# Kernel tuning notes

Measured on AMD Instinct MI355X. Metric: run time of the kernel, lower is better.

Reference implementation:

```python
import jax, jax.numpy as jnp
import numpy as np

N = 1024      # num_waves
L = 32        # latent_dim
H = 64        # hidden_dim
EPS = 1e-6
SELF_SCALE = 0.5
INT_SCALE = 0.3


def _xavier(k, shape, gain=0.5):
    fan_out, fan_in = shape
    std = gain * np.sqrt(2.0 / (fan_in + fan_out))
    return (jax.random.normal(k, shape, jnp.float32) * std).astype(jnp.float32)


def setup_inputs() -> dict:
    key = jax.random.key(0)
    ks = jax.random.split(key, 12)
    d = {}
    d['state'] = jax.random.normal(ks[0], (N * (L + 1),), jnp.float32)
    # SelfDynamicsNetwork: L->H->H->L, tanh, xavier_normal gain=0.5, zero bias
    d['Ws1'] = _xavier(ks[1], (H, L)); d['bs1'] = jnp.zeros((H,), jnp.float32)
    d['Ws2'] = _xavier(ks[2], (H, H)); d['bs2'] = jnp.zeros((H,), jnp.float32)
    d['Ws3'] = _xavier(ks[3], (L, H)); d['bs3'] = jnp.zeros((L,), jnp.float32)
    # InteractionNetwork: 4L->H->H->L
    d['Wi1'] = _xavier(ks[4], (H, 4 * L)); d['bi1'] = jnp.zeros((H,), jnp.float32)
    d['Wi2'] = _xavier(ks[5], (H, H));     d['bi2'] = jnp.zeros((H,), jnp.float32)
    d['Wi3'] = _xavier(ks[6], (L, H));     d['bi3'] = jnp.zeros((L,), jnp.float32)
    # QuantumPhaseMixer
    d['phase_w'] = jax.random.normal(ks[7], (L,), jnp.float32) * 0.1
    d['Wc'] = _xavier(ks[8], (L, 2 * L), gain=1.0)
    d['bc'] = jnp.zeros((L,), jnp.float32)
    # per-wave aggressiveness
    d['aggr'] = jnp.ones((N,), jnp.float32) * 0.5
    return d


def reference(state, Ws1, bs1, Ws2, bs2, Ws3, bs3,
              Wi1, bi1, Wi2, bi2, Wi3, bi3,
              phase_w, Wc, bc, aggr):
    s = state.reshape(N, L + 1)
    h = s[:, :L]          # [N, L]
    phases = s[:, L]      # [N]

    def mlp(x, W1, b1, W2, b2, W3, b3):
        x = jnp.tanh(x @ W1.T + b1)
        x = jnp.tanh(x @ W2.T + b2)
        return x @ W3.T + b3

    self_term = mlp(h, Ws1, bs1, Ws2, bs2, Ws3, bs3)   # [N, L]
    dh = self_term  # prev_state is None -> estimated velocity = self_dynamics(h)

    # pairwise distance factor
    diff = h[:, None, :] - h[None, :, :]                # [N, N, L] (h_i - h_j)
    dist = jnp.linalg.norm(diff, axis=-1) + EPS         # [N, N]
    dfac = jnp.minimum(1.0 / dist, 2.0)

    # InteractionNetwork on concat([h_i, h_j, dh_i, dh_j]): split first layer
    a_i = h @ Wi1[:, :L].T + dh @ Wi1[:, 2 * L:3 * L].T           # [N, H]
    b_j = h @ Wi1[:, L:2 * L].T + dh @ Wi1[:, 3 * L:].T + bi1    # [N, H]
    x1 = jnp.tanh(a_i[:, None, :] + b_j[None, :, :])              # [N, N, H]
    x2 = jnp.tanh(x1 @ Wi2.T + bi2)                               # [N, N, H]
    k_ij = x2 @ Wi3.T + bi3                                       # [N, N, L]

    # QuantumPhaseMixer
    phase_diff = phases[:, None] - phases[None, :]                # [N, N]
    pf = jnp.cos(phase_diff[..., None] * phase_w)                 # [N, N, L]
    coh = jax.nn.sigmoid((h @ Wc[:, :L].T)[:, None, :]
                         + (h @ Wc[:, L:].T)[None, :, :] + bc)    # [N, N, L]
    quantum = pf * coh * (-diff)                                  # h_j - h_i = -diff

    agg = jax.nn.sigmoid(aggr)                                    # [N]
    inter = dfac[..., None] * k_ij * agg[:, None, None] + quantum # [N, N, L]
    mask = 1.0 - jnp.eye(N, dtype=inter.dtype)                    # skip j == i
    isum = jnp.einsum('ijl,ij->il', inter, mask)                  # sum over j

    # env is None -> speed_mults = 1, refractions = 0
    dh_dt = SELF_SCALE * self_term + INT_SCALE * isum
    dphase = 0.1 + 0.05 * jnp.sum(jnp.abs(isum), axis=-1)
    return jnp.concatenate([dh_dt, dphase[:, None]], axis=1).reshape(-1)
```

## Files before the change

### kernel.cpp

```cpp
#include <hip/hip_runtime.h>
#include <hip/hip_bf16.h>
#include <math.h>

#define NN 1024
#define LDIM 32
#define HDIM 64

#define WS_SELF 0
#define WS_AA   (WS_SELF + NN*LDIM)
#define WS_CI   (WS_AA   + NN*HDIM)
#define WS_AGG  (WS_CI   + NN*LDIM)
#define WS_BI2  (WS_AGG  + NN)
#define WS_BI3  (WS_BI2  + HDIM)
#define WS_FEND (WS_BI3  + LDIM)

#define U_BJB  0
#define U_HJB  (U_BJB + NN*HDIM)
#define U_JT   (U_HJB + NN*LDIM)
#define U_W2B  (U_JT  + NN*LDIM*4)
#define U_W3B  (U_W2B + HDIM*HDIM)
#define U_END  (U_W3B + LDIM*HDIM)

#define PK_W1  0
#define PK_W2  1024
#define PK_W3  3072
#define PK_WI1 4096
#define PK_WC  8192
#define PK_END 9216

#define K2P  2.88539008f
#define K1N  (-1.44269504f)

typedef __attribute__((ext_vector_type(8))) short bf16x8;
typedef __attribute__((ext_vector_type(4))) float f32x4;

__device__ __forceinline__ float fast_rcp(float x) { return __builtin_amdgcn_rcpf(x); }
__device__ __forceinline__ float fast_tanh(float x) {
    float e = __builtin_amdgcn_exp2f(x * K2P);
    return 1.0f - 2.0f * fast_rcp(e + 1.0f);
}
__device__ __forceinline__ float tanh_pre(float xp) {
    return 1.0f - 2.0f * fast_rcp(__builtin_amdgcn_exp2f(xp) + 1.0f);
}
__device__ __forceinline__ float fast_sigmoid(float x) {
    return fast_rcp(1.0f + __builtin_amdgcn_exp2f(x * K1N));
}
__device__ __forceinline__ float blo(unsigned int u) { union { unsigned int i; float f; } v; v.i = u << 16; return v.f; }
__device__ __forceinline__ float bhi(unsigned int u) { union { unsigned int i; float f; } v; v.i = u & 0xffff0000u; return v.f; }
__device__ __forceinline__ float bf2f(unsigned short u) { union { unsigned int i; float f; } v; v.i = ((unsigned int)u) << 16; return v.f; }
__device__ __forceinline__ unsigned short f2bf(float f) {
    __hip_bfloat16 b = __float2bfloat16(f);
    unsigned short u; __builtin_memcpy(&u, &b, 2); return u;
}
__device__ __forceinline__ unsigned int pk2(float a, float b) {
    float2 t; t.x = a; t.y = b;
    __hip_bfloat162 h = __float22bfloat162_rn(t);
    unsigned int u; __builtin_memcpy(&u, &h, 4); return u;
}

__global__ __launch_bounds__(256) void precompute(
    const float* __restrict__ state,
    const float* __restrict__ Ws1, const float* __restrict__ bs1,
    const float* __restrict__ Ws2, const float* __restrict__ bs2,
    const float* __restrict__ Ws3, const float* __restrict__ bs3,
    const float* __restrict__ Wi1, const float* __restrict__ bi1,
    const float* __restrict__ Wi2, const float* __restrict__ bi2,
    const float* __restrict__ Wi3, const float* __restrict__ bi3,
    const float* __restrict__ phw, const float* __restrict__ Wc,
    const float* __restrict__ bc,  const float* __restrict__ aggr,
    float* __restrict__ ws, unsigned short* __restrict__ wsu) {
    const int tid = threadIdx.x;
    const int w = tid >> 6, t = tid & 63;
    const int i = blockIdx.x * 4 + w;

    __shared__ unsigned int wlds[PK_END];
    __shared__ float shh[4][32], shdh[4][32], sht1[4][64], sht2[4][64];
    __shared__ float shph[4];

    {
        const float2* s1 = (const float2*)Ws1;
        #pragma unroll
        for (int r = 0; r < 4; r++) { int e = tid + r * 256; int f = e >> 4, k2 = e & 15;
            float2 v = s1[e]; wlds[PK_W1 + k2 * 64 + f] = pk2(v.x, v.y); }
        const float2* s2 = (const float2*)Ws2;
        #pragma unroll
        for (int r = 0; r < 8; r++) { int e = tid + r * 256; int f = e >> 5, k2 = e & 31;
            float2 v = s2[e]; wlds[PK_W2 + k2 * 64 + f] = pk2(v.x, v.y); }
        const float2* s3 = (const float2*)Ws3;
        #pragma unroll
        for (int r = 0; r < 4; r++) { int e = tid + r * 256; int f = e >> 5, k2 = e & 31;
            float2 v = s3[e]; wlds[PK_W3 + k2 * 32 + f] = pk2(v.x, v.y); }
        const float2* si = (const float2*)Wi1;
        #pragma unroll
        for (int r = 0; r < 16; r++) { int e = tid + r * 256; int f = e >> 6, c2 = e & 63;
            float2 v = si[e]; wlds[PK_WI1 + c2 * 64 + f] = pk2(v.x, v.y); }
        const float2* sc = (const float2*)Wc;
        #pragma unroll
        for (int r = 0; r < 4; r++) { int e = tid + r * 256; int f = e >> 5, c2 = e & 31;
            float2 v = sc[e]; wlds[PK_WC + c2 * 32 + f] = pk2(v.x, v.y); }
    }
    if (blockIdx.x == 0) {
        #pragma unroll
        for (int r = 0; r < 16; r++) { int e = tid + r * 256; wsu[U_W2B + e] = f2bf(Wi2[e] * K2P); }
        #pragma unroll
        for (int r = 0; r < 8; r++)  { int e = tid + r * 256; wsu[U_W3B + e] = f2bf(Wi3[e]); }
        if (tid < HDIM) ws[WS_BI2 + tid] = bi2[tid] * K2P;
        if (tid < LDIM) ws[WS_BI3 + tid] = bi3[tid];
    }

    float sv = (t < 33) ? state[i * 33 + t] : 0.f;
    if (t < 32) shh[w][t] = sv;
    if (t == 32) shph[w] = sv;
    if (t == 33) ws[WS_AGG + i] = fast_sigmoid(aggr[i]);
    __syncthreads();

    {
        float s = bs1[t];
        const unsigned int* W = wlds + PK_W1;
        #pragma unroll
        for (int k2 = 0; k2 < 16; k2++) {
            unsigned int p = W[k2 * 64 + t];
            s = fmaf(blo(p), shh[w][2 * k2], s);
            s = fmaf(bhi(p), shh[w][2 * k2 + 1], s);
        }
        sht1[w][t] = fast_tanh(s);
    }
    __syncthreads();
    {
        float s = bs2[t];
        const unsigned int* W = wlds + PK_W2;
        #pragma unroll
        for (int k2 = 0; k2 < 32; k2++) {
            unsigned int p = W[k2 * 64 + t];
            s = fmaf(blo(p), sht1[w][2 * k2], s);
            s = fmaf(bhi(p), sht1[w][2 * k2 + 1], s);
        }
        sht2[w][t] = fast_tanh(s);
    }
    __syncthreads();
    if (t < 32) {
        float s = bs3[t];
        const unsigned int* W = wlds + PK_W3;
        #pragma unroll
        for (int k2 = 0; k2 < 32; k2++) {
            unsigned int p = W[k2 * 32 + t];
            s = fmaf(blo(p), sht2[w][2 * k2], s);
            s = fmaf(bhi(p), sht2[w][2 * k2 + 1], s);
        }
        ws[WS_SELF + i * 32 + t] = s;
        shdh[w][t] = s;
    }
    __syncthreads();
    {
        float sa = 0.f, sb = bi1[t];
        const unsigned int* W = wlds + PK_WI1;
        #pragma unroll
        for (int k2 = 0; k2 < 16; k2++) {
            float h0 = shh[w][2 * k2], h1 = shh[w][2 * k2 + 1];
            float d0 = shdh[w][2 * k2], d1 = shdh[w][2 * k2 + 1];
            unsigned int wa  = W[k2 * 64 + t];
            unsigned int wb  = W[(16 + k2) * 64 + t];
            unsigned int wa2 = W[(32 + k2) * 64 + t];
            unsigned int wb2 = W[(48 + k2) * 64 + t];
            sa = fmaf(blo(wa), h0, sa);  sa = fmaf(bhi(wa), h1, sa);
            sb = fmaf(blo(wb), h0, sb);  sb = fmaf(bhi(wb), h1, sb);
            sa = fmaf(blo(wa2), d0, sa); sa = fmaf(bhi(wa2), d1, sa);
            sb = fmaf(blo(wb2), d0, sb); sb = fmaf(bhi(wb2), d1, sb);
        }
        ws[WS_AA + i * 64 + t]  = sa * K2P;
        wsu[U_BJB + i * 64 + t] = f2bf(sb * K2P);
    }
    if (t < 32) {
        float si = 0.f, sj = 0.f;
        const unsigned int* W = wlds + PK_WC;
        #pragma unroll
        for (int m2 = 0; m2 < 16; m2++) {
            float h0 = shh[w][2 * m2], h1 = shh[w][2 * m2 + 1];
            unsigned int wi = W[m2 * 32 + t];
            unsigned int wj = W[(16 + m2) * 32 + t];
            si = fmaf(blo(wi), h0, si); si = fmaf(bhi(wi), h1, si);
            sj = fmaf(blo(wj), h0, sj); sj = fmaf(bhi(wj), h1, sj);
        }
        ws[WS_CI + i * 32 + t] = (si + bc[t]) * K1N;
        float h = shh[w][t];
        wsu[U_HJB + i * 32 + t] = f2bf(h);
        float sc, cc;
        __sincosf(shph[w] * phw[t], &sc, &cc);
        uint2 jt; jt.x = pk2(h, sj * K1N); jt.y = pk2(cc, sc);
        *(uint2*)(wsu + U_JT + (i * 32 + t) * 4) = jt;
    }
}

__global__ __launch_bounds__(256) void pair_kernel(
    const float* __restrict__ ws, const unsigned short* __restrict__ wsu,
    float* __restrict__ out) {
    const int i    = blockIdx.x;
    const int tid  = threadIdx.x;
    const int w    = tid >> 6;
    const int lane = tid & 63;
    const int q    = lane >> 4;
    const int m    = lane & 15;
    const int jw   = w * 16;
    const int sub  = lane & 3;

    __shared__ unsigned short W2ls[64 * 72];
    __shared__ unsigned short W3ls[32 * 72];
    __shared__ unsigned short x2ls[4 * 2 * 16 * 72];
    __shared__ float aLS[64];
    __shared__ float redT[4][32], redU[4][32], redV[4][32];
    __shared__ float sfw[4];

    if (tid < 64) aLS[tid] = ws[WS_AA + i * 64 + tid];
    {
        int row = tid >> 2, c = (tid & 3) * 16;
        const uint4* s2 = (const uint4*)(wsu + U_W2B + row * 64 + c);
        uint4 d0 = s2[0], d1 = s2[1];
        uint4* dd = (uint4*)(&W2ls[row * 72 + c]);
        dd[0] = d0; dd[1] = d1;
        if (row < 32) {
            const uint4* s3 = (const uint4*)(wsu + U_W3B + row * 64 + c);
            uint4 e0 = s3[0], e1 = s3[1];
            uint4* d3 = (uint4*)(&W3ls[row * 72 + c]);
            d3[0] = e0; d3[1] = e1;
        }
    }
    float hi8[8];
    {
        uint4 hv4 = *(const uint4*)(wsu + U_HJB + i * 32 + sub * 8);
        unsigned int hd[4] = {hv4.x, hv4.y, hv4.z, hv4.w};
        #pragma unroll
        for (int e = 0; e < 4; e++) { hi8[2 * e] = blo(hd[e]); hi8[2 * e + 1] = bhi(hd[e]); }
    }
    f32x4 b2q[4];
    #pragma unroll
    for (int nb = 0; nb < 4; nb++) {
        float4 bv = *(const float4*)(ws + WS_BI2 + nb * 16 + q * 4);
        b2q[nb][0] = bv.x; b2q[nb][1] = bv.y; b2q[nb][2] = bv.z; b2q[nb][3] = bv.w;
    }
    float hiv[2], cibv[2];
    #pragma unroll
    for (int lb = 0; lb < 2; lb++) {
        int l = lb * 16 + m;
        hiv[lb]  = bf2f(wsu[U_HJB + i * 32 + l]);
        cibv[lb] = ws[WS_CI + i * 32 + l];
    }
    const float aggi = ws[WS_AGG + i];
    const float sub0 = (sub == 0) ? 1.0f : 0.0f;

    const unsigned short* hp = wsu + U_HJB + (jw + (lane >> 2)) * 32 + sub * 8;
    const unsigned short* bp = wsu + U_BJB + (jw + m) * 64 + q * 8;
    const unsigned short* jp = wsu + U_JT + ((jw + q * 4) * 32 + m) * 4;

    uint4 hvA = *(const uint4*)hp;
    uint4 b0A = *(const uint4*)bp;
    uint4 b1A = *(const uint4*)(bp + 32);
    uint4 hvB, b0B, b1B;
    __syncthreads();

    f32x4 accK[2];
    #pragma unroll
    for (int lb = 0; lb < 2; lb++) { accK[lb][0]=0.f; accK[lb][1]=0.f; accK[lb][2]=0.f; accK[lb][3]=0.f; }
    float aU[2] = {0.f, 0.f}, aV[2] = {0.f, 0.f};
    float sumfac = 0.f;

    unsigned short* xb0 = &x2ls[w * 2 * 1152];
    unsigned short* xb1 = xb0 + 1152;

    auto stageB = [&](const unsigned short* xb) {
        bf16x8 x2f[2];
        #pragma unroll
        for (int s = 0; s < 2; s++)
            x2f[s] = *(const bf16x8*)(&xb[m * 72 + s * 32 + q * 8]);
        #pragma unroll
        for (int lb = 0; lb < 2; lb++) {
            #pragma unroll
            for (int s = 0; s < 2; s++) {
                bf16x8 w3f = *(const bf16x8*)(&W3ls[(lb * 16 + m) * 72 + s * 32 + q * 8]);
                accK[lb] = __builtin_amdgcn_mfma_f32_16x16x32_bf16(x2f[s], w3f, accK[lb], 0, 0, 0);
            }
        }
    };

    auto body = [&](int T, uint4 hvc, uint4 b0c, uint4 b1c,
                    uint4& hvn, uint4& b0n, uint4& b1n,
                    unsigned short* xcur, const unsigned short* xprev) {
        hp += 2048; bp += 4096;
        hvn = *(const uint4*)hp;
        b0n = *(const uint4*)bp;
        b1n = *(const uint4*)(bp + 32);
        uint2 jt[8];
        #pragma unroll
        for (int r = 0; r < 4; r++) {
            jt[r]     = *(const uint2*)(jp + r * 128);
            jt[4 + r] = *(const uint2*)(jp + 64 + r * 128);
        }
        jp += 8192;

        if (T > 0) stageB(xprev);

        float facm;
        {
            unsigned int hd[4] = {hvc.x, hvc.y, hvc.z, hvc.w};
            float s = 0.f;
            #pragma unroll
            for (int e = 0; e < 4; e++) {
                float d0 = hi8[2 * e]     - blo(hd[e]);
                float d1 = hi8[2 * e + 1] - bhi(hd[e]);
                s = fmaf(d0, d0, s); s = fmaf(d1, d1, s);
            }
            s += __shfl_xor(s, 1); s += __shfl_xor(s, 2);
            int jj = T * 64 + jw + (lane >> 2);
            float facown = fminf(__builtin_amdgcn_rsqf(s), 2.0f) * aggi;
            facown = (jj == i) ? 0.0f : facown;
            sumfac = fmaf(sub0, facown, sumfac);
            facm = __shfl(facown, 4 * m);
        }
        const float fm2 = -2.0f * facm;

        bf16x8 afr[2];
        {
            unsigned int bd[8] = {b0c.x, b0c.y, b0c.z, b0c.w, b1c.x, b1c.y, b1c.z, b1c.w};
            #pragma unroll
            for (int s = 0; s < 2; s++) {
                union { uint4 u4; bf16x8 v; } pkd;
                #pragma unroll
                for (int e = 0; e < 4; e++) {
                    const float* ab = &aLS[s * 32 + q * 8 + 2 * e];
                    float x0 = tanh_pre(ab[0] + blo(bd[s * 4 + e]));
                    float x1 = tanh_pre(ab[1] + bhi(bd[s * 4 + e]));
                    ((unsigned int*)&pkd.u4)[e] = pk2(x0, x1);
                }
                afr[s] = pkd.v;
            }
        }

        f32x4 accA[4];
        #pragma unroll
        for (int nb = 0; nb < 4; nb++) {
            f32x4 acc = b2q[nb];
            #pragma unroll
            for (int s = 0; s < 2; s++) {
                bf16x8 w2f = *(const bf16x8*)(&W2ls[(nb * 16 + m) * 72 + s * 32 + q * 8]);
                acc = __builtin_amdgcn_mfma_f32_16x16x32_bf16(w2f, afr[s], acc, 0, 0, 0);
            }
            accA[nb] = acc;
        }
        #pragma unroll
        for (int nb = 0; nb < 4; nb++) {
            float r0 = fast_rcp(__builtin_amdgcn_exp2f(accA[nb][0]) + 1.0f);
            float r1 = fast_rcp(__builtin_amdgcn_exp2f(accA[nb][1]) + 1.0f);
            float r2 = fast_rcp(__builtin_amdgcn_exp2f(accA[nb][2]) + 1.0f);
            float r3 = fast_rcp(__builtin_amdgcn_exp2f(accA[nb][3]) + 1.0f);
            float t0 = fmaf(fm2, r0, facm), t1 = fmaf(fm2, r1, facm);
            float t2 = fmaf(fm2, r2, facm), t3 = fmaf(fm2, r3, facm);
            uint2 pk; pk.x = pk2(t0, t1); pk.y = pk2(t2, t3);
            *(uint2*)(&xcur[m * 72 + nb * 16 + q * 4]) = pk;
        }

        #pragma unroll
        for (int lb = 0; lb < 2; lb++) {
            float u = 0.f, v = 0.f;
            #pragma unroll
            for (int r = 0; r < 4; r++) {
                uint2 jv = jt[lb * 4 + r];
                float hj = blo(jv.x), cj = bhi(jv.x);
                float pjc = blo(jv.y), pjs = bhi(jv.y);
                float coh = fast_rcp(1.0f + __builtin_amdgcn_exp2f(cibv[lb] + cj));
                float cd  = coh * (hiv[lb] - hj);
                u = fmaf(cd, pjc, u);
                v = fmaf(cd, pjs, v);
            }
            aU[lb] += u; aV[lb] += v;
        }
    };

    #pragma unroll 1
    for (int T = 0; T < 16; T += 2) {
        body(T,     hvA, b0A, b1A, hvB, b0B, b1B, xb0, xb1);
        body(T + 1, hvB, b0B, b1B, hvA, b0A, b1A, xb1, xb0);
    }
    stageB(xb1);

    float T1[2];
    #pragma unroll
    for (int lb = 0; lb < 2; lb++) {
        T1[lb] = (accK[lb][0] + accK[lb][1]) + (accK[lb][2] + accK[lb][3]);
        T1[lb] += __shfl_xor(T1[lb], 16); T1[lb] += __shfl_xor(T1[lb], 32);
        aU[lb] += __shfl_xor(aU[lb], 16); aU[lb] += __shfl_xor(aU[lb], 32);
        aV[lb] += __shfl_xor(aV[lb], 16); aV[lb] += __shfl_xor(aV[lb], 32);
    }
    sumfac += __shfl_xor(sumfac, 1);  sumfac += __shfl_xor(sumfac, 2);
    sumfac += __shfl_xor(sumfac, 4);  sumfac += __shfl_xor(sumfac, 8);
    sumfac += __shfl_xor(sumfac, 16); sumfac += __shfl_xor(sumfac, 32);
    if (lane < 16) {
        redT[w][m] = T1[0];      redT[w][16 + m] = T1[1];
        redU[w][m] = aU[0];      redU[w][16 + m] = aU[1];
        redV[w][m] = aV[0];      redV[w][16 + m] = aV[1];
    }
    if (lane == 0) sfw[w] = sumfac;
    __syncthreads();
    if (tid < 32) {
        int l = tid;
        float t1 = (redT[0][l] + redT[1][l]) + (redT[2][l] + redT[3][l]);
        float uu = (redU[0][l] + redU[1][l]) + (redU[2][l] + redU[3][l]);
        float vv = (redV[0][l] + redV[1][l]) + (redV[2][l] + redV[3][l]);
        float sf = (sfw[0] + sfw[1]) + (sfw[2] + sfw[3]);
        uint2 jti = *(const uint2*)(wsu + U_JT + (i * 32 + l) * 4);
        float pic = blo(jti.y), pis = bhi(jti.y);
        float isum = t1 + sf * ws[WS_BI3 + l] - (pic * uu + pis * vv);
        out[i * 33 + l] = 0.5f * ws[WS_SELF + i * 32 + l] + 0.3f * isum;
        redT[0][l] = fabsf(isum);
    }
    __syncthreads();
    if (tid == 0) {
        float s = 0.f;
        #pragma unroll
        for (int l = 0; l < 32; l++) s += redT[0][l];
        out[i * 33 + 32] = 0.1f + 0.05f * s;
    }
}

extern "C" void kernel_launch(void* const* d_in, const int* in_sizes, int n_in,
                              void* d_out, int out_size, void* d_ws, size_t ws_size,
                              hipStream_t stream) {
    const float* state   = (const float*)d_in[0];
    const float* Ws1     = (const float*)d_in[1];
    const float* bs1     = (const float*)d_in[2];
    const float* Ws2     = (const float*)d_in[3];
    const float* bs2     = (const float*)d_in[4];
    const float* Ws3     = (const float*)d_in[5];
    const float* bs3     = (const float*)d_in[6];
    const float* Wi1     = (const float*)d_in[7];
    const float* bi1     = (const float*)d_in[8];
    const float* Wi2     = (const float*)d_in[9];
    const float* bi2     = (const float*)d_in[10];
    const float* Wi3     = (const float*)d_in[11];
    const float* bi3     = (const float*)d_in[12];
    const float* phase_w = (const float*)d_in[13];
    const float* Wc      = (const float*)d_in[14];
    const float* bc      = (const float*)d_in[15];
    const float* aggr    = (const float*)d_in[16];

    float* ws = (float*)d_ws;
    unsigned short* wsu = (unsigned short*)(ws + WS_FEND);
    float* out = (float*)d_out;

    precompute<<<256, 256, 0, stream>>>(state, Ws1, bs1, Ws2, bs2, Ws3, bs3,
                                        Wi1, bi1, Wi2, bi2, Wi3, bi3,
                                        phase_w, Wc, bc, aggr, ws, wsu);
    pair_kernel<<<NN, 256, 0, stream>>>(ws, wsu, out);
}
```

Baseline: 150.6 us.

## Split pair kernel over j halves with atomic partials and finalize kernel

Each row i's j-range is now split across two blocks (grid 1024x2). Partial sums are accumulated into a workspace with atomicAdd, and a new finalize kernel computes the outputs. The W3 fragments move from LDS into registers, and the double-buffered register/LDS software pipeline is dropped in favour of a single buffer. The aim is more blocks for better occupancy and load balance, at the cost of a memset, an extra launch, float atomics and lost prefetch overlap.

```diff
diff --git a/kernel.cpp b/kernel.cpp
--- a/kernel.cpp
+++ b/kernel.cpp
@@ -12,7 +12,8 @@
 #define WS_AGG  (WS_CI   + NN*LDIM)
 #define WS_BI2  (WS_AGG  + NN)
 #define WS_BI3  (WS_BI2  + HDIM)
-#define WS_FEND (WS_BI3  + LDIM)
+#define WS_PT   (WS_BI3  + LDIM)
+#define WS_FEND (WS_PT   + NN*100)
 
 #define U_BJB  0
 #define U_HJB  (U_BJB + NN*HDIM)
@@ -193,8 +194,9 @@
 
 __global__ __launch_bounds__(256) void pair_kernel(
     const float* __restrict__ ws, const unsigned short* __restrict__ wsu,
-    float* __restrict__ out) {
+    float* __restrict__ wsmut) {
     const int i    = blockIdx.x;
+    const int j0   = blockIdx.y << 9;
     const int tid  = threadIdx.x;
     const int w    = tid >> 6;
     const int lane = tid & 63;
@@ -204,8 +206,7 @@
     const int sub  = lane & 3;
 
     __shared__ unsigned short W2ls[64 * 72];
-    __shared__ unsigned short W3ls[32 * 72];
-    __shared__ unsigned short x2ls[4 * 2 * 16 * 72];
+    __shared__ unsigned short x2ls[4 * 16 * 72];
     __shared__ float aLS[64];
     __shared__ float redT[4][32], redU[4][32], redV[4][32];
     __shared__ float sfw[4];
@@ -217,12 +218,6 @@
         uint4 d0 = s2[0], d1 = s2[1];
         uint4* dd = (uint4*)(&W2ls[row * 72 + c]);
         dd[0] = d0; dd[1] = d1;
-        if (row < 32) {
-            const uint4* s3 = (const uint4*)(wsu + U_W3B + row * 64 + c);
-            uint4 e0 = s3[0], e1 = s3[1];
-            uint4* d3 = (uint4*)(&W3ls[row * 72 + c]);
-            d3[0] = e0; d3[1] = e1;
-        }
     }
     float hi8[8];
     {
@@ -237,6 +232,12 @@
         float4 bv = *(const float4*)(ws + WS_BI2 + nb * 16 + q * 4);
         b2q[nb][0] = bv.x; b2q[nb][1] = bv.y; b2q[nb][2] = bv.z; b2q[nb][3] = bv.w;
     }
+    bf16x8 w3f[2][2];
+    #pragma unroll
+    for (int lb = 0; lb < 2; lb++)
+        #pragma unroll
+        for (int s = 0; s < 2; s++)
+            w3f[lb][s] = *(const bf16x8*)(wsu + U_W3B + (lb * 16 + m) * 64 + s * 32 + q * 8);
     float hiv[2], cibv[2];
     #pragma unroll
     for (int lb = 0; lb < 2; lb++) {
@@ -247,14 +248,9 @@
     const float aggi = ws[WS_AGG + i];
     const float sub0 = (sub == 0) ? 1.0f : 0.0f;
 
-    const unsigned short* hp = wsu + U_HJB + (jw + (lane >> 2)) * 32 + sub * 8;
-    const unsigned short* bp = wsu + U_BJB + (jw + m) * 64 + q * 8;
-    const unsigned short* jp = wsu + U_JT + ((jw + q * 4) * 32 + m) * 4;
-
-    uint4 hvA = *(const uint4*)hp;
-    uint4 b0A = *(const uint4*)bp;
-    uint4 b1A = *(const uint4*)(bp + 32);
-    uint4 hvB, b0B, b1B;
+    const unsigned short* hp = wsu + U_HJB + (j0 + jw + (lane >> 2)) * 32 + sub * 8;
+    const unsigned short* bp = wsu + U_BJB + (j0 + jw + m) * 64 + q * 8;
+    const unsigned short* jp = wsu + U_JT + ((j0 + jw + q * 4) * 32 + m) * 4;
     __syncthreads();
 
     f32x4 accK[2];
@@ -263,31 +259,13 @@
     float aU[2] = {0.f, 0.f}, aV[2] = {0.f, 0.f};
     float sumfac = 0.f;
 
-    unsigned short* xb0 = &x2ls[w * 2 * 1152];
-    unsigned short* xb1 = xb0 + 1152;
-
-    auto stageB = [&](const unsigned short* xb) {
-        bf16x8 x2f[2];
-        #pragma unroll
-        for (int s = 0; s < 2; s++)
-            x2f[s] = *(const bf16x8*)(&xb[m * 72 + s * 32 + q * 8]);
-        #pragma unroll
-        for (int lb = 0; lb < 2; lb++) {
-            #pragma unroll
-            for (int s = 0; s < 2; s++) {
-                bf16x8 w3f = *(const bf16x8*)(&W3ls[(lb * 16 + m) * 72 + s * 32 + q * 8]);
-                accK[lb] = __builtin_amdgcn_mfma_f32_16x16x32_bf16(x2f[s], w3f, accK[lb], 0, 0, 0);
-            }
-        }
-    };
-
-    auto body = [&](int T, uint4 hvc, uint4 b0c, uint4 b1c,
-                    uint4& hvn, uint4& b0n, uint4& b1n,
-                    unsigned short* xcur, const unsigned short* xprev) {
-        hp += 2048; bp += 4096;
-        hvn = *(const uint4*)hp;
-        b0n = *(const uint4*)bp;
-        b1n = *(const uint4*)(bp + 32);
+    unsigned short* xw = &x2ls[w * 1152];
+
+    #pragma unroll 1
+    for (int T = 0; T < 8; T++) {
+        uint4 hv = *(const uint4*)hp;  hp += 2048;
+        uint4 b0 = *(const uint4*)bp;
+        uint4 b1 = *(const uint4*)(bp + 32);  bp += 4096;
         uint2 jt[8];
         #pragma unroll
         for (int r = 0; r < 4; r++) {
@@ -296,11 +274,22 @@
         }
         jp += 8192;
 
-        if (T > 0) stageB(xprev);
+        if (T > 0) {
+            bf16x8 x2f[2];
+            #pragma unroll
+            for (int s = 0; s < 2; s++)
+                x2f[s] = *(const bf16x8*)(&xw[m * 72 + s * 32 + q * 8]);
+            #pragma unroll
+            for (int lb = 0; lb < 2; lb++) {
+                #pragma unroll
+                for (int s = 0; s < 2; s++)
+                    accK[lb] = __builtin_amdgcn_mfma_f32_16x16x32_bf16(x2f[s], w3f[lb][s], accK[lb], 0, 0, 0);
+            }
+        }
 
         float facm;
         {
-            unsigned int hd[4] = {hvc.x, hvc.y, hvc.z, hvc.w};
+            unsigned int hd[4] = {hv.x, hv.y, hv.z, hv.w};
             float s = 0.f;
             #pragma unroll
             for (int e = 0; e < 4; e++) {
@@ -309,7 +298,7 @@
                 s = fmaf(d0, d0, s); s = fmaf(d1, d1, s);
             }
             s += __shfl_xor(s, 1); s += __shfl_xor(s, 2);
-            int jj = T * 64 + jw + (lane >> 2);
+            int jj = j0 + T * 64 + jw + (lane >> 2);
             float facown = fminf(__builtin_amdgcn_rsqf(s), 2.0f) * aggi;
             facown = (jj == i) ? 0.0f : facown;
             sumfac = fmaf(sub0, facown, sumfac);
@@ -319,7 +308,7 @@
 
         bf16x8 afr[2];
         {
-            unsigned int bd[8] = {b0c.x, b0c.y, b0c.z, b0c.w, b1c.x, b1c.y, b1c.z, b1c.w};
+            unsigned int bd[8] = {b0.x, b0.y, b0.z, b0.w, b1.x, b1.y, b1.z, b1.w};
             #pragma unroll
             for (int s = 0; s < 2; s++) {
                 union { uint4 u4; bf16x8 v; } pkd;
@@ -354,7 +343,7 @@
             float t0 = fmaf(fm2, r0, facm), t1 = fmaf(fm2, r1, facm);
             float t2 = fmaf(fm2, r2, facm), t3 = fmaf(fm2, r3, facm);
             uint2 pk; pk.x = pk2(t0, t1); pk.y = pk2(t2, t3);
-            *(uint2*)(&xcur[m * 72 + nb * 16 + q * 4]) = pk;
+            *(uint2*)(&xw[m * 72 + nb * 16 + q * 4]) = pk;
         }
 
         #pragma unroll
@@ -372,14 +361,19 @@
             }
             aU[lb] += u; aV[lb] += v;
         }
-    };
-
-    #pragma unroll 1
-    for (int T = 0; T < 16; T += 2) {
-        body(T,     hvA, b0A, b1A, hvB, b0B, b1B, xb0, xb1);
-        body(T + 1, hvB, b0B, b1B, hvA, b0A, b1A, xb1, xb0);
-    }
-    stageB(xb1);
+    }
+    {
+        bf16x8 x2f[2];
+        #pragma unroll
+        for (int s = 0; s < 2; s++)
+            x2f[s] = *(const bf16x8*)(&xw[m * 72 + s * 32 + q * 8]);
+        #pragma unroll
+        for (int lb = 0; lb < 2; lb++) {
+            #pragma unroll
+            for (int s = 0; s < 2; s++)
+                accK[lb] = __builtin_amdgcn_mfma_f32_16x16x32_bf16(x2f[s], w3f[lb][s], accK[lb], 0, 0, 0);
+        }
+    }
 
     float T1[2];
     #pragma unroll
@@ -399,25 +393,33 @@
     }
     if (lane == 0) sfw[w] = sumfac;
     __syncthreads();
+    float* PT = wsmut + WS_PT + i * 100;
     if (tid < 32) {
         int l = tid;
-        float t1 = (redT[0][l] + redT[1][l]) + (redT[2][l] + redT[3][l]);
-        float uu = (redU[0][l] + redU[1][l]) + (redU[2][l] + redU[3][l]);
-        float vv = (redV[0][l] + redV[1][l]) + (redV[2][l] + redV[3][l]);
-        float sf = (sfw[0] + sfw[1]) + (sfw[2] + sfw[3]);
-        uint2 jti = *(const uint2*)(wsu + U_JT + (i * 32 + l) * 4);
+        atomicAdd(&PT[l],      (redT[0][l] + redT[1][l]) + (redT[2][l] + redT[3][l]));
+        atomicAdd(&PT[32 + l], (redU[0][l] + redU[1][l]) + (redU[2][l] + redU[3][l]));
+        atomicAdd(&PT[64 + l], (redV[0][l] + redV[1][l]) + (redV[2][l] + redV[3][l]));
+    }
+    if (tid == 0) atomicAdd(&PT[96], (sfw[0] + sfw[1]) + (sfw[2] + sfw[3]));
+}
+
+__global__ __launch_bounds__(64) void finalize(
+    const float* __restrict__ ws, const unsigned short* __restrict__ wsu,
+    float* __restrict__ out) {
+    const int i = blockIdx.x, t = threadIdx.x;
+    float a = 0.f;
+    if (t < 32) {
+        const float* PT = ws + WS_PT + i * 100;
+        float t1 = PT[t], uu = PT[32 + t], vv = PT[64 + t], sf = PT[96];
+        uint2 jti = *(const uint2*)(wsu + U_JT + (i * 32 + t) * 4);
         float pic = blo(jti.y), pis = bhi(jti.y);
-        float isum = t1 + sf * ws[WS_BI3 + l] - (pic * uu + pis * vv);
-        out[i * 33 + l] = 0.5f * ws[WS_SELF + i * 32 + l] + 0.3f * isum;
-        redT[0][l] = fabsf(isum);
-    }
-    __syncthreads();
-    if (tid == 0) {
-        float s = 0.f;
-        #pragma unroll
-        for (int l = 0; l < 32; l++) s += redT[0][l];
-        out[i * 33 + 32] = 0.1f + 0.05f * s;
-    }
+        float isum = t1 + sf * ws[WS_BI3 + t] - (pic * uu + pis * vv);
+        out[i * 33 + t] = 0.5f * ws[WS_SELF + i * 32 + t] + 0.3f * isum;
+        a = fabsf(isum);
+    }
+    a += __shfl_xor(a, 1);  a += __shfl_xor(a, 2);  a += __shfl_xor(a, 4);
+    a += __shfl_xor(a, 8);  a += __shfl_xor(a, 16); a += __shfl_xor(a, 32);
+    if (t == 0) out[i * 33 + 32] = 0.1f + 0.05f * a;
 }
 
 extern "C" void kernel_launch(void* const* d_in, const int* in_sizes, int n_in,
@@ -445,8 +447,11 @@
     unsigned short* wsu = (unsigned short*)(ws + WS_FEND);
     float* out = (float*)d_out;
 
+    hipMemsetAsync(ws + WS_PT, 0, NN * 100 * sizeof(float), stream);
+
     precompute<<<256, 256, 0, stream>>>(state, Ws1, bs1, Ws2, bs2, Ws3, bs3,
                                         Wi1, bi1, Wi2, bi2, Wi3, bi3,
                                         phase_w, Wc, bc, aggr, ws, wsu);
-    pair_kernel<<<NN, 256, 0, stream>>>(ws, wsu, out);
-}
+    pair_kernel<<<dim3(NN, 2), 256, 0, stream>>>(ws, wsu, ws);
+    finalize<<<NN, 64, 0, stream>>>(ws, wsu, out);
+}
```

Result: slower. 158.0 us (+4.9%).

## Precompute pairwise distance factors in a separate kernel, store as bf16 matrix

Applied to the files above, without the earlier changes.

Moves the pairwise distance factor computation (squared norm, rsqrt, clamp, aggr scaling, diagonal mask) out of the pair kernel into a new fac_kernel. That kernel writes an NxN bf16 matrix to workspace, which the pair kernel then loads per tile. This removes the per-tile h_j loads, FMAs and cross-lane shuffles from the hot loop, but adds a kernel launch and a 2 MB round trip through global memory. The factor is also rounded to bf16.

```diff
diff --git a/kernel.cpp b/kernel.cpp
--- a/kernel.cpp
+++ b/kernel.cpp
@@ -19,7 +19,8 @@
 #define U_JT   (U_HJB + NN*LDIM)
 #define U_W2B  (U_JT  + NN*LDIM*4)
 #define U_W3B  (U_W2B + HDIM*HDIM)
-#define U_END  (U_W3B + LDIM*HDIM)
+#define U_FAC  (U_W3B + LDIM*HDIM)
+#define U_END  (U_FAC + NN*NN)
 
 #define PK_W1  0
 #define PK_W2  1024
@@ -191,6 +192,36 @@
     }
 }
 
+__global__ __launch_bounds__(256) void fac_kernel(
+    const float* __restrict__ ws, unsigned short* __restrict__ wsu) {
+    const int i = blockIdx.x, tid = threadIdx.x;
+    __shared__ float hi[32];
+    __shared__ float ag[1];
+    if (tid < 32) hi[tid] = bf2f(wsu[U_HJB + i * 32 + tid]);
+    if (tid == 32) ag[0] = ws[WS_AGG + i];
+    __syncthreads();
+    const float agg = ag[0];
+    #pragma unroll
+    for (int r = 0; r < 4; r++) {
+        int j = tid + r * 256;
+        const uint4* hj = (const uint4*)(wsu + U_HJB + j * 32);
+        float s = 0.f;
+        #pragma unroll
+        for (int v4 = 0; v4 < 4; v4++) {
+            uint4 hv = hj[v4];
+            unsigned int hd[4] = {hv.x, hv.y, hv.z, hv.w};
+            #pragma unroll
+            for (int e = 0; e < 4; e++) {
+                float d0 = hi[v4 * 8 + 2 * e]     - blo(hd[e]);
+                float d1 = hi[v4 * 8 + 2 * e + 1] - bhi(hd[e]);
+                s = fmaf(d0, d0, s); s = fmaf(d1, d1, s);
+            }
+        }
+        float f = fminf(__builtin_amdgcn_rsqf(s), 2.0f) * agg;
+        wsu[U_FAC + i * 1024 + j] = (j == i) ? (unsigned short)0 : f2bf(f);
+    }
+}
+
 __global__ __launch_bounds__(256) void pair_kernel(
     const float* __restrict__ ws, const unsigned short* __restrict__ wsu,
     float* __restrict__ out) {
@@ -201,7 +232,6 @@
     const int q    = lane >> 4;
     const int m    = lane & 15;
     const int jw   = w * 16;
-    const int sub  = lane & 3;
 
     __shared__ unsigned short W2ls[64 * 72];
     __shared__ unsigned short W3ls[32 * 72];
@@ -224,13 +254,6 @@
             d3[0] = e0; d3[1] = e1;
         }
     }
-    float hi8[8];
-    {
-        uint4 hv4 = *(const uint4*)(wsu + U_HJB + i * 32 + sub * 8);
-        unsigned int hd[4] = {hv4.x, hv4.y, hv4.z, hv4.w};
-        #pragma unroll
-        for (int e = 0; e < 4; e++) { hi8[2 * e] = blo(hd[e]); hi8[2 * e + 1] = bhi(hd[e]); }
-    }
     f32x4 b2q[4];
     #pragma unroll
     for (int nb = 0; nb < 4; nb++) {
@@ -244,17 +267,15 @@
         hiv[lb]  = bf2f(wsu[U_HJB + i * 32 + l]);
         cibv[lb] = ws[WS_CI + i * 32 + l];
     }
-    const float aggi = ws[WS_AGG + i];
-    const float sub0 = (sub == 0) ? 1.0f : 0.0f;
-
-    const unsigned short* hp = wsu + U_HJB + (jw + (lane >> 2)) * 32 + sub * 8;
+    const float q0 = (q == 0) ? 1.0f : 0.0f;
+
     const unsigned short* bp = wsu + U_BJB + (jw + m) * 64 + q * 8;
     const unsigned short* jp = wsu + U_JT + ((jw + q * 4) * 32 + m) * 4;
-
-    uint4 hvA = *(const uint4*)hp;
+    const unsigned short* fp = wsu + U_FAC + i * 1024 + jw;
+
     uint4 b0A = *(const uint4*)bp;
     uint4 b1A = *(const uint4*)(bp + 32);
-    uint4 hvB, b0B, b1B;
+    uint4 b0B, b1B;
     __syncthreads();
 
     f32x4 accK[2];
@@ -281,13 +302,13 @@
         }
     };
 
-    auto body = [&](int T, uint4 hvc, uint4 b0c, uint4 b1c,
-                    uint4& hvn, uint4& b0n, uint4& b1n,
+    auto body = [&](int T, uint4 b0c, uint4 b1c,
+                    uint4& b0n, uint4& b1n,
                     unsigned short* xcur, const unsigned short* xprev) {
-        hp += 2048; bp += 4096;
-        hvn = *(const uint4*)hp;
+        bp += 4096;
         b0n = *(const uint4*)bp;
         b1n = *(const uint4*)(bp + 32);
+        float facm = bf2f(fp[m]);  fp += 64;
         uint2 jt[8];
         #pragma unroll
         for (int r = 0; r < 4; r++) {
@@ -298,23 +319,7 @@
 
         if (T > 0) stageB(xprev);
 
-        float facm;
-        {
-            unsigned int hd[4] = {hvc.x, hvc.y, hvc.z, hvc.w};
-            float s = 0.f;
-            #pragma unroll
-            for (int e = 0; e < 4; e++) {
-                float d0 = hi8[2 * e]     - blo(hd[e]);
-                float d1 = hi8[2 * e + 1] - bhi(hd[e]);
-                s = fmaf(d0, d0, s); s = fmaf(d1, d1, s);
-            }
-            s += __shfl_xor(s, 1); s += __shfl_xor(s, 2);
-            int jj = T * 64 + jw + (lane >> 2);
-            float facown = fminf(__builtin_amdgcn_rsqf(s), 2.0f) * aggi;
-            facown = (jj == i) ? 0.0f : facown;
-            sumfac = fmaf(sub0, facown, sumfac);
-            facm = __shfl(facown, 4 * m);
-        }
+        sumfac = fmaf(q0, facm, sumfac);
         const float fm2 = -2.0f * facm;
 
         bf16x8 afr[2];
@@ -376,8 +381,8 @@
 
     #pragma unroll 1
     for (int T = 0; T < 16; T += 2) {
-        body(T,     hvA, b0A, b1A, hvB, b0B, b1B, xb0, xb1);
-        body(T + 1, hvB, b0B, b1B, hvA, b0A, b1A, xb1, xb0);
+        body(T,     b0A, b1A, b0B, b1B, xb0, xb1);
+        body(T + 1, b0B, b1B, b0A, b1A, xb1, xb0);
     }
     stageB(xb1);
 
@@ -448,5 +453,6 @@
     precompute<<<256, 256, 0, stream>>>(state, Ws1, bs1, Ws2, bs2, Ws3, bs3,
                                         Wi1, bi1, Wi2, bi2, Wi3, bi3,
                                         phase_w, Wc, bc, aggr, ws, wsu);
+    fac_kernel<<<NN, 256, 0, stream>>>(ws, wsu);
     pair_kernel<<<NN, 256, 0, stream>>>(ws, wsu, out);
 }
```

Measured after the change: 156.9 us. 4.2% more time.

## Process two j-tiles per iteration with interleaved MFMA stages instead of register prefetch

Applied to the files above, without the earlier changes.

Restructures the main loop so each iteration loads and processes two 64-wide j tiles together: both distance factors, both tanh fragment builds, both MFMA stage-A chains, then stage B and the coherence stage. The explicit cross-iteration register double-buffering of global loads is removed. Instead, more independent work sits inside one iteration so the scheduler can overlap MFMA and transcendental latency. In exchange, global loads are no longer prefetched one tile ahead, and holding two tiles of state raises register pressure.

```diff
diff --git a/kernel.cpp b/kernel.cpp
--- a/kernel.cpp
+++ b/kernel.cpp
@@ -250,11 +250,6 @@
     const unsigned short* hp = wsu + U_HJB + (jw + (lane >> 2)) * 32 + sub * 8;
     const unsigned short* bp = wsu + U_BJB + (jw + m) * 64 + q * 8;
     const unsigned short* jp = wsu + U_JT + ((jw + q * 4) * 32 + m) * 4;
-
-    uint4 hvA = *(const uint4*)hp;
-    uint4 b0A = *(const uint4*)bp;
-    uint4 b1A = *(const uint4*)(bp + 32);
-    uint4 hvB, b0B, b1B;
     __syncthreads();
 
     f32x4 accK[2];
@@ -281,60 +276,23 @@
         }
     };
 
-    auto body = [&](int T, uint4 hvc, uint4 b0c, uint4 b1c,
-                    uint4& hvn, uint4& b0n, uint4& b1n,
-                    unsigned short* xcur, const unsigned short* xprev) {
-        hp += 2048; bp += 4096;
-        hvn = *(const uint4*)hp;
-        b0n = *(const uint4*)bp;
-        b1n = *(const uint4*)(bp + 32);
-        uint2 jt[8];
-        #pragma unroll
-        for (int r = 0; r < 4; r++) {
-            jt[r]     = *(const uint2*)(jp + r * 128);
-            jt[4 + r] = *(const uint2*)(jp + 64 + r * 128);
-        }
-        jp += 8192;
-
-        if (T > 0) stageB(xprev);
-
-        float facm;
-        {
-            unsigned int hd[4] = {hvc.x, hvc.y, hvc.z, hvc.w};
-            float s = 0.f;
+    auto buildAfr = [&](uint4 bA, uint4 bB, bf16x8* afr) {
+        unsigned int bd[8] = {bA.x, bA.y, bA.z, bA.w, bB.x, bB.y, bB.z, bB.w};
+        #pragma unroll
+        for (int s = 0; s < 2; s++) {
+            union { uint4 u4; bf16x8 v; } pkd;
             #pragma unroll
             for (int e = 0; e < 4; e++) {
-                float d0 = hi8[2 * e]     - blo(hd[e]);
-                float d1 = hi8[2 * e + 1] - bhi(hd[e]);
-                s = fmaf(d0, d0, s); s = fmaf(d1, d1, s);
+                const float* ab = &aLS[s * 32 + q * 8 + 2 * e];
+                float x0 = tanh_pre(ab[0] + blo(bd[s * 4 + e]));
+                float x1 = tanh_pre(ab[1] + bhi(bd[s * 4 + e]));
+                ((unsigned int*)&pkd.u4)[e] = pk2(x0, x1);
             }
-            s += __shfl_xor(s, 1); s += __shfl_xor(s, 2);
-            int jj = T * 64 + jw + (lane >> 2);
-            float facown = fminf(__builtin_amdgcn_rsqf(s), 2.0f) * aggi;
-            facown = (jj == i) ? 0.0f : facown;
-            sumfac = fmaf(sub0, facown, sumfac);
-            facm = __shfl(facown, 4 * m);
-        }
-        const float fm2 = -2.0f * facm;
-
-        bf16x8 afr[2];
-        {
-            unsigned int bd[8] = {b0c.x, b0c.y, b0c.z, b0c.w, b1c.x, b1c.y, b1c.z, b1c.w};
-            #pragma unroll
-            for (int s = 0; s < 2; s++) {
-                union { uint4 u4; bf16x8 v; } pkd;
-                #pragma unroll
-                for (int e = 0; e < 4; e++) {
-                    const float* ab = &aLS[s * 32 + q * 8 + 2 * e];
-                    float x0 = tanh_pre(ab[0] + blo(bd[s * 4 + e]));
-                    float x1 = tanh_pre(ab[1] + bhi(bd[s * 4 + e]));
-                    ((unsigned int*)&pkd.u4)[e] = pk2(x0, x1);
-                }
-                afr[s] = pkd.v;
-            }
-        }
-
-        f32x4 accA[4];
+            afr[s] = pkd.v;
+        }
+    };
+
+    auto stageA = [&](const bf16x8* afr, f32x4* accA) {
         #pragma unroll
         for (int nb = 0; nb < 4; nb++) {
             f32x4 acc = b2q[nb];
@@ -345,6 +303,10 @@
             }
             accA[nb] = acc;
         }
+    };
+
+    auto epiA = [&](const f32x4* accA, float facm, unsigned short* xcur) {
+        const float fm2 = -2.0f * facm;
         #pragma unroll
         for (int nb = 0; nb < 4; nb++) {
             float r0 = fast_rcp(__builtin_amdgcn_exp2f(accA[nb][0]) + 1.0f);
@@ -356,7 +318,9 @@
             uint2 pk; pk.x = pk2(t0, t1); pk.y = pk2(t2, t3);
             *(uint2*)(&xcur[m * 72 + nb * 16 + q * 4]) = pk;
         }
-
+    };
+
+    auto stageC = [&](const uint2* jt) {
         #pragma unroll
         for (int lb = 0; lb < 2; lb++) {
             float u = 0.f, v = 0.f;
@@ -374,10 +338,69 @@
         }
     };
 
+    auto facOf = [&](uint4 hv, int jj) -> float {
+        unsigned int hd[4] = {hv.x, hv.y, hv.z, hv.w};
+        float s = 0.f;
+        #pragma unroll
+        for (int e = 0; e < 4; e++) {
+            float d0 = hi8[2 * e]     - blo(hd[e]);
+            float d1 = hi8[2 * e + 1] - bhi(hd[e]);
+            s = fmaf(d0, d0, s); s = fmaf(d1, d1, s);
+        }
+        s += __shfl_xor(s, 1); s += __shfl_xor(s, 2);
+        float f = fminf(__builtin_amdgcn_rsqf(s), 2.0f) * aggi;
+        return (jj == i) ? 0.0f : f;
+    };
+
     #pragma unroll 1
-    for (int T = 0; T < 16; T += 2) {
-        body(T,     hvA, b0A, b1A, hvB, b0B, b1B, xb0, xb1);
-        body(T + 1, hvB, b0B, b1B, hvA, b0A, b1A, xb1, xb0);
+    for (int TP = 0; TP < 16; TP += 2) {
+        uint4 hv0 = *(const uint4*)hp;
+        uint4 hv1 = *(const uint4*)(hp + 2048);
+        hp += 4096;
+        uint4 b00 = *(const uint4*)bp;
+        uint4 b01 = *(const uint4*)(bp + 32);
+        uint4 b10 = *(const uint4*)(bp + 4096);
+        uint4 b11 = *(const uint4*)(bp + 4128);
+        bp += 8192;
+        uint2 jt0[8];
+        #pragma unroll
+        for (int r = 0; r < 4; r++) {
+            jt0[r]     = *(const uint2*)(jp + r * 128);
+            jt0[4 + r] = *(const uint2*)(jp + 64 + r * 128);
+        }
+
+        if (TP > 0) stageB(xb1);
+
+        int jj0 = TP * 64 + jw + (lane >> 2);
+        float f0 = facOf(hv0, jj0);
+        float f1 = facOf(hv1, jj0 + 64);
+        sumfac = fmaf(sub0, f0, sumfac);
+        sumfac = fmaf(sub0, f1, sumfac);
+        float facm0 = __shfl(f0, 4 * m);
+        float facm1 = __shfl(f1, 4 * m);
+
+        bf16x8 afr0[2], afr1[2];
+        buildAfr(b00, b01, afr0);
+        buildAfr(b10, b11, afr1);
+
+        f32x4 accA0[4], accA1[4];
+        stageA(afr0, accA0);
+        stageA(afr1, accA1);
+
+        epiA(accA0, facm0, xb0);
+        epiA(accA1, facm1, xb1);
+
+        stageB(xb0);
+
+        stageC(jt0);
+        uint2 jt1[8];
+        #pragma unroll
+        for (int r = 0; r < 4; r++) {
+            jt1[r]     = *(const uint2*)(jp + 8192 + r * 128);
+            jt1[4 + r] = *(const uint2*)(jp + 8192 + 64 + r * 128);
+        }
+        jp += 16384;
+        stageC(jt1);
     }
     stageB(xb1);
 
```

Result: no change. 152.6 us (+1.3%).
